# Performance work log

Measured on AMD Instinct MI355X. Metric: run time of the kernel, lower is better.

The kernel has to match this reference:

```python
import jax, jax.numpy as jnp
import numpy as np


def _mlp(x, w1, b1, w2, b2):
    # torch Mlp: fc1 -> GELU (exact erf) -> fc2, dropout off in eval
    h = jax.nn.gelu(x @ w1 + b1, approximate=False)
    return h @ w2 + b2


def _nearest(x, oh, ow):
    # torch F.interpolate mode='nearest' on [B,h,w,d]: src = floor(dst*in/out)
    h, w = x.shape[1], x.shape[2]
    ih = (np.arange(oh) * h) // oh
    iw = (np.arange(ow) * w) // ow
    return x[:, ih][:, :, iw]


def setup_inputs() -> dict:
    key = jax.random.key(0)
    ks = jax.random.split(key, 8)
    B, s0, dim, nPnt, new2 = 4, 12, 256, 128, 48  # new_size=24
    sc = 0.02
    return {
        "token_init": jax.random.normal(ks[0], (B, s0, s0, dim), jnp.float32),
        "point_token": jax.random.normal(ks[1], (B, nPnt, dim), jnp.float32),
        "nr_w1": jax.random.normal(ks[2], (nPnt, 4 * nPnt), jnp.float32) * sc,
        "nr_b1": jnp.zeros((4 * nPnt,), jnp.float32),
        "nr_w2": jax.random.normal(ks[3], (4 * nPnt, nPnt), jnp.float32) * sc,
        "nr_b2": jnp.zeros((nPnt,), jnp.float32),
        "na_w1": jax.random.normal(ks[4], (nPnt, 4 * nPnt), jnp.float32) * sc,
        "na_b1": jnp.zeros((4 * nPnt,), jnp.float32),
        "na_w2": jax.random.normal(ks[5], (4 * nPnt, nPnt), jnp.float32) * sc,
        "na_b2": jnp.zeros((nPnt,), jnp.float32),
        "tf_w1": jax.random.normal(ks[6], (new2, new2), jnp.float32) * sc,
        "tf_b1": jnp.zeros((new2,), jnp.float32),
        "tf_w2": jax.random.normal(ks[7], (new2, 1), jnp.float32) * sc,
        "tf_b2": jnp.zeros((1,), jnp.float32),
        "height": 120,
        "width": 160,
    }


def reference(token_init, point_token, nr_w1, nr_b1, nr_w2, nr_b2,
              na_w1, na_b1, na_w2, na_b2, tf_w1, tf_b1, tf_w2, tf_b2,
              height, width):
    B, nPnt, dim = point_token.shape
    new_size = tf_w1.shape[0] // 2
    scale = dim ** (-0.5)
    # is_init=False path: repeat_interleave x2 along H and W
    t = jnp.repeat(jnp.repeat(token_init, 2, axis=1), 2, axis=2)  # [B,2s,2s,d]
    token_raw = _nearest(t, height, width)                        # [B,H,W,d]
    t_exp = _nearest(t, new_size, new_size)                       # [B,sH,sW,d]
    sH = sW = new_size
    token_templ = t_exp.reshape(B, sH * sW, dim)
    node_adj = jnp.einsum('bnd,bpd->bnp', token_templ, point_token) * scale
    node_adj = _mlp(node_adj, nr_w1, nr_b1, nr_w2, nr_b2)
    node_adj = node_adj.reshape(B, sH, sW, nPnt)
    node_w = jnp.einsum('bhwp,bhwd->bhpd', node_adj, t_exp) * (sW ** -0.5)
    node_h = jnp.einsum('bhwp,bhwd->bwpd', node_adj, t_exp) * (sH ** -0.5)
    token_n = jnp.concatenate([node_w, node_h], axis=1)           # [B,2s,nPnt,d]
    x = token_n.reshape(B, sH + sW, nPnt * dim).transpose(0, 2, 1)  # [B,nPnt*d,2s]
    token_fused = _mlp(x, tf_w1, tf_b1, tf_w2, tf_b2)             # [B,nPnt*d,1]
    token_fused = token_fused.reshape(B, nPnt, dim)
    token_raw_f = token_raw.reshape(B, height * width, dim)
    node_attn = jnp.einsum('bnd,bpd->bnp', token_raw_f, point_token) * scale
    node_attn = jax.nn.softmax(_mlp(node_attn, na_w1, na_b1, na_w2, na_b2), axis=-1)
    token_new = node_attn @ token_fused + token_raw_f             # [B,HW,d]
    return token_new
```

## Files before the change

kernel.cpp:

```cpp
#include <hip/hip_runtime.h>
#include <math.h>

#define B     4
#define DIM   256
#define NP    128
#define NS    144
#define HID   512
#define NROW  576
#define H_OUT 120
#define W_OUT 160

__device__ __forceinline__ float gelu_exact(float x) {
    return 0.5f * x * (1.0f + erff(x * 0.70710678118654752440f));
}

__global__ __launch_bounds__(256) void k_t(
    const float* __restrict__ pt, float* __restrict__ ptT)
{
    const int bid = blockIdx.x;
    const int b   = bid >> 5;
    const int rem = bid & 31;
    const int d0  = (rem >> 2) * 32;
    const int p0  = (rem & 3) * 32;
    const int t   = threadIdx.x;
    __shared__ float tile[32][33];

    #pragma unroll
    for (int i = t; i < 1024; i += 256) {
        const int row = i >> 5, col = i & 31;
        tile[row][col] = pt[(size_t)(b * NP + p0 + row) * DIM + d0 + col];
    }
    __syncthreads();
    #pragma unroll
    for (int i = t; i < 1024; i += 256) {
        const int row = i >> 5, col = i & 31;
        ptT[(size_t)(b * DIM + d0 + row) * NP + p0 + col] = tile[col][row];
    }
}

__global__ __launch_bounds__(256) void k_mlp(
    const float* __restrict__ ti, const float* __restrict__ ptT,
    const float* __restrict__ nr_w1, const float* __restrict__ nr_b1,
    const float* __restrict__ nr_w2, const float* __restrict__ nr_b2,
    const float* __restrict__ na_w1, const float* __restrict__ na_b1,
    const float* __restrict__ na_w2, const float* __restrict__ na_b2,
    float* __restrict__ nadjT, float* __restrict__ attn)
{
    const int mlp  = blockIdx.x / 144;
    const int tile = blockIdx.x % 144;
    const int g0 = tile * 4;
    const int b  = g0 / NS;
    const int n0 = g0 % NS;
    const int t  = threadIdx.x;

    const float* __restrict__ w1 = mlp ? na_w1 : nr_w1;
    const float* __restrict__ b1 = mlp ? na_b1 : nr_b1;
    const float* __restrict__ w2 = mlp ? na_w2 : nr_w2;
    const float* __restrict__ b2 = mlp ? na_b2 : nr_b2;

    __shared__ float xs[4][DIM];
    __shared__ float parA[2][4][NP];
    __shared__ float qs[4][NP];
    __shared__ float hs[4][HID];
    __shared__ float par[8][4][NP];
    __shared__ float wred[4][2];

    {
        const int r = t >> 6, c = t & 63;
        ((float4*)xs[r])[c] = ((const float4*)ti)[(size_t)(g0 + r) * 64 + c];
    }
    __syncthreads();

    {
        const int pq = t & 31;
        const int rr = (t >> 5) & 3;
        const int dh = t >> 7;
        const float4* __restrict__ pT4 =
            (const float4*)(ptT + (size_t)b * DIM * NP) + pq;
        float4 acc = make_float4(0.f, 0.f, 0.f, 0.f);
        #pragma unroll 8
        for (int d2 = 0; d2 < 128; ++d2) {
            const int d = dh * 128 + d2;
            const float4 v4 = pT4[(size_t)d * 32];
            const float  xv = xs[rr][d];
            acc.x += xv * v4.x; acc.y += xv * v4.y;
            acc.z += xv * v4.z; acc.w += xv * v4.w;
        }
        ((float4*)parA[dh][rr])[pq] = acc;
    }
    __syncthreads();

    const int p  = t & 127;
    const int rh = t >> 7;
    qs[rh][p]     = (parA[0][rh][p]     + parA[1][rh][p])     * 0.0625f;
    qs[rh + 2][p] = (parA[0][rh + 2][p] + parA[1][rh + 2][p]) * 0.0625f;
    __syncthreads();

    {
        const int kq = t & 127;
        const int k0 = kq * 4;
        float4 acc0 = *(const float4*)(b1 + k0);
        float4 acc1 = acc0;
        const float* __restrict__ wp = w1 + k0;
        #pragma unroll 16
        for (int pp = 0; pp < NP; ++pp) {
            const float4 w4 = *(const float4*)(wp + (size_t)pp * HID);
            const float q0 = qs[rh][pp];
            const float q1 = qs[rh + 2][pp];
            acc0.x += q0*w4.x; acc0.y += q0*w4.y;
            acc0.z += q0*w4.z; acc0.w += q0*w4.w;
            acc1.x += q1*w4.x; acc1.y += q1*w4.y;
            acc1.z += q1*w4.z; acc1.w += q1*w4.w;
        }
        float4 o0, o1;
        o0.x = gelu_exact(acc0.x); o0.y = gelu_exact(acc0.y);
        o0.z = gelu_exact(acc0.z); o0.w = gelu_exact(acc0.w);
        o1.x = gelu_exact(acc1.x); o1.y = gelu_exact(acc1.y);
        o1.z = gelu_exact(acc1.z); o1.w = gelu_exact(acc1.w);
        ((float4*)hs[rh])[kq]     = o0;
        ((float4*)hs[rh + 2])[kq] = o1;
    }
    __syncthreads();

    {
        const int pq = t & 31;
        const int p0 = pq * 4;
        const int kg = t >> 5;
        float4 a0 = make_float4(0.f,0.f,0.f,0.f);
        float4 a1 = a0, a2 = a0, a3 = a0;
        const float4* __restrict__ w24 = (const float4*)(w2 + p0);
        #pragma unroll 8
        for (int i = 0; i < 64; ++i) {
            const int k = kg * 64 + i;
            const float4 w4 = w24[(size_t)k * 32];
            const float h0 = hs[0][k], h1 = hs[1][k];
            const float h2 = hs[2][k], h3 = hs[3][k];
            a0.x += h0*w4.x; a0.y += h0*w4.y; a0.z += h0*w4.z; a0.w += h0*w4.w;
            a1.x += h1*w4.x; a1.y += h1*w4.y; a1.z += h1*w4.z; a1.w += h1*w4.w;
            a2.x += h2*w4.x; a2.y += h2*w4.y; a2.z += h2*w4.z; a2.w += h2*w4.w;
            a3.x += h3*w4.x; a3.y += h3*w4.y; a3.z += h3*w4.z; a3.w += h3*w4.w;
        }
        ((float4*)par[kg][0])[pq] = a0;
        ((float4*)par[kg][1])[pq] = a1;
        ((float4*)par[kg][2])[pq] = a2;
        ((float4*)par[kg][3])[pq] = a3;
    }
    __syncthreads();

    float lg0 = b2[p], lg1 = lg0;
    #pragma unroll
    for (int kg = 0; kg < 8; ++kg) {
        lg0 += par[kg][rh][p];
        lg1 += par[kg][rh + 2][p];
    }

    if (mlp == 0) {
        float* __restrict__ dst = nadjT + (size_t)(b * NP + p) * NS + n0;
        dst[rh]     = lg0;
        dst[rh + 2] = lg1;
    } else {
        const int wid   = t >> 6;
        const int wpair = wid ^ 1;
        float m0 = lg0, m1 = lg1;
        #pragma unroll
        for (int off = 32; off > 0; off >>= 1) {
            m0 = fmaxf(m0, __shfl_xor(m0, off));
            m1 = fmaxf(m1, __shfl_xor(m1, off));
        }
        if ((t & 63) == 0) { wred[wid][0] = m0; wred[wid][1] = m1; }
        __syncthreads();
        m0 = fmaxf(m0, wred[wpair][0]);
        m1 = fmaxf(m1, wred[wpair][1]);

        const float e0 = expf(lg0 - m0), e1 = expf(lg1 - m1);
        float s0 = e0, s1 = e1;
        #pragma unroll
        for (int off = 32; off > 0; off >>= 1) {
            s0 += __shfl_xor(s0, off);
            s1 += __shfl_xor(s1, off);
        }
        __syncthreads();
        if ((t & 63) == 0) { wred[wid][0] = s0; wred[wid][1] = s1; }
        __syncthreads();
        s0 += wred[wpair][0];
        s1 += wred[wpair][1];

        attn[(size_t)(g0 + rh) * NP + p]     = e0 / s0;
        attn[(size_t)(g0 + rh + 2) * NP + p] = e1 / s1;
    }
}

__global__ __launch_bounds__(256) void k_fold(
    const float* __restrict__ nadjT, const float* __restrict__ ti,
    const float* __restrict__ w1, const float* __restrict__ b1,
    const float* __restrict__ w2, const float* __restrict__ b2,
    float* __restrict__ tf)
{
    const int b = blockIdx.x >> 7;
    const int p = blockIdx.x & 127;
    const int t = threadIdx.x;
    __shared__ float an[NS];
    __shared__ float w1p[24][48];
    __shared__ float b1s[48];
    __shared__ float w2s[48];

    if (t < 36) {
        ((float4*)an)[t] =
            ((const float4*)(nadjT + (size_t)(b * NP + p) * NS))[t];
    }
    if (t >= 192 && t < 240) {
        const int k = t - 192;
        b1s[k] = b1[k];
        w2s[k] = w2[k];
    }
    for (int i = t; i < 24 * 48; i += 256) {
        const int m = i / 48, k = i - m * 48;
        w1p[m][k] = w1[(2 * m) * 48 + k] + w1[(2 * m + 1) * 48 + k];
    }
    __syncthreads();

    const int d = t;
    const float* __restrict__ tb = ti + (size_t)b * NS * DIM + d;
    float v[24];
    #pragma unroll
    for (int m = 0; m < 24; ++m) v[m] = 0.f;
    #pragma unroll
    for (int y = 0; y < 12; ++y) {
        #pragma unroll
        for (int x = 0; x < 12; ++x) {
            const int n = y * 12 + x;
            const float tv = tb[n * DIM];
            const float a  = an[n];
            v[y]      += a * tv;
            v[12 + x] += a * tv;
        }
    }
    const float c = 0.40824829046386301637f;
    #pragma unroll
    for (int m = 0; m < 24; ++m) v[m] *= c;

    float acc = b2[0];
    for (int k = 0; k < 48; ++k) {
        float tt = b1s[k];
        #pragma unroll
        for (int m = 0; m < 24; ++m) tt += v[m] * w1p[m][k];
        acc += gelu_exact(tt) * w2s[k];
    }
    tf[(size_t)(b * NP + p) * DIM + d] = acc;
}

__global__ __launch_bounds__(256) void k_final(
    const float* __restrict__ attn, const float* __restrict__ tf,
    const float* __restrict__ ti, float4* __restrict__ out)
{
    const int g = blockIdx.x;
    const int b = g / NS;
    const int n = g % NS;
    const int t = threadIdx.x;
    const int dq = t & 63;
    const int pg = t >> 6;

    __shared__ float  at[NP];
    __shared__ float4 par4[4][64];
    __shared__ float4 rowf[64];

    if (t < NP) at[t] = attn[(size_t)g * NP + t];
    __syncthreads();

    const float4* __restrict__ tp = (const float4*)tf + (size_t)b * NP * 64 + dq;
    float4 acc = make_float4(0.f, 0.f, 0.f, 0.f);
    #pragma unroll 16
    for (int i = 0; i < 32; ++i) {
        const int pp = pg * 32 + i;
        const float  a  = at[pp];
        const float4 tv = tp[(size_t)pp * 64];
        acc.x += a * tv.x; acc.y += a * tv.y;
        acc.z += a * tv.z; acc.w += a * tv.w;
    }
    par4[pg][dq] = acc;
    __syncthreads();

    if (t < 64) {
        float4 s = par4[0][t];
        const float4 s1 = par4[1][t], s2 = par4[2][t], s3 = par4[3][t];
        const float4 tiv = ((const float4*)ti)[(size_t)g * 64 + t];
        s.x += s1.x + s2.x + s3.x + tiv.x;
        s.y += s1.y + s2.y + s3.y + tiv.y;
        s.z += s1.z + s2.z + s3.z + tiv.z;
        s.w += s1.w + s2.w + s3.w + tiv.w;
        rowf[t] = s;
    }
    __syncthreads();

    const int y = n / 12, x = n % 12;
    const int w_lo = (40 * x + 2) / 3;
    const int w_hi = (40 * x + 42) / 3;
    const float4 val = rowf[dq];
    const int h0 = 10 * y;
    for (int h = h0; h < h0 + 10; ++h) {
        float4* __restrict__ orow = out + (size_t)((b * H_OUT + h) * W_OUT) * 64 + dq;
        for (int w = w_lo + pg; w < w_hi; w += 4) {
            orow[(size_t)w * 64] = val;
        }
    }
}

extern "C" void kernel_launch(void* const* d_in, const int* in_sizes, int n_in,
                              void* d_out, int out_size, void* d_ws, size_t ws_size,
                              hipStream_t stream) {
    (void)in_sizes; (void)n_in; (void)out_size; (void)ws_size;
    const float* token_init  = (const float*)d_in[0];
    const float* point_token = (const float*)d_in[1];
    const float* nr_w1 = (const float*)d_in[2];
    const float* nr_b1 = (const float*)d_in[3];
    const float* nr_w2 = (const float*)d_in[4];
    const float* nr_b2 = (const float*)d_in[5];
    const float* na_w1 = (const float*)d_in[6];
    const float* na_b1 = (const float*)d_in[7];
    const float* na_w2 = (const float*)d_in[8];
    const float* na_b2 = (const float*)d_in[9];
    const float* tf_w1 = (const float*)d_in[10];
    const float* tf_b1 = (const float*)d_in[11];
    const float* tf_w2 = (const float*)d_in[12];
    const float* tf_b2 = (const float*)d_in[13];

    float* out = (float*)d_out;
    float* ws  = (float*)d_ws;
    float* nadjT = ws;
    float* attn  = nadjT + NROW * NP;
    float* tf    = attn + NROW * NP;
    float* ptT   = tf + B * NP * DIM;

    k_t<<<128, 256, 0, stream>>>(point_token, ptT);
    k_mlp<<<288, 256, 0, stream>>>(token_init, ptT,
                                   nr_w1, nr_b1, nr_w2, nr_b2,
                                   na_w1, na_b1, na_w2, na_b2,
                                   nadjT, attn);
    k_fold<<<B * NP, 256, 0, stream>>>(nadjT, token_init,
                                       tf_w1, tf_b1, tf_w2, tf_b2, tf);
    k_final<<<NROW, 256, 0, stream>>>(attn, tf, token_init, (float4*)out);
}
```

Measured before the change: 166.9 us.

## Precompute folded tf_w1 once and register-block the score GEMV over rows

The row-pair sum of tf_w1 used by k_fold is now computed once by an extra block in the transpose kernel and stored in workspace. This replaces the 512 per-block shared-memory rebuilds, and k_fold now reads weights, biases and node_adj straight from global memory with no barrier. In k_mlp the point-token score product now has each thread compute all 4 rows over a 32-wide slice of d, so each ptT float4 load is reused across 4 rows. The cost is an 8-way partial reduction instead of a 2-way one. The global weight reads in k_fold go through cache instead of shared memory, which may add latency in the inner GELU loop.

Measured after the change: 160.7 us. -3.7%, faster.

```diff
diff --git a/kernel.cpp b/kernel.cpp
--- a/kernel.cpp
+++ b/kernel.cpp
@@ -15,14 +15,24 @@
 }
 
 __global__ __launch_bounds__(256) void k_t(
-    const float* __restrict__ pt, float* __restrict__ ptT)
+    const float* __restrict__ pt, const float* __restrict__ tf_w1,
+    float* __restrict__ ptT, float* __restrict__ w1pg)
 {
     const int bid = blockIdx.x;
+    const int t   = threadIdx.x;
+
+    if (bid == 128) {
+        for (int i = t; i < 24 * 48; i += 256) {
+            const int m = i / 48, k = i - m * 48;
+            w1pg[i] = tf_w1[(2 * m) * 48 + k] + tf_w1[(2 * m + 1) * 48 + k];
+        }
+        return;
+    }
+
     const int b   = bid >> 5;
     const int rem = bid & 31;
     const int d0  = (rem >> 2) * 32;
     const int p0  = (rem & 3) * 32;
-    const int t   = threadIdx.x;
     __shared__ float tile[32][33];
 
     #pragma unroll
@@ -59,7 +69,7 @@
     const float* __restrict__ b2 = mlp ? na_b2 : nr_b2;
 
     __shared__ float xs[4][DIM];
-    __shared__ float parA[2][4][NP];
+    __shared__ float parA[8][4][NP];
     __shared__ float qs[4][NP];
     __shared__ float hs[4][HID];
     __shared__ float par[8][4][NP];
@@ -73,27 +83,41 @@
 
     {
         const int pq = t & 31;
-        const int rr = (t >> 5) & 3;
-        const int dh = t >> 7;
+        const int dg = t >> 5;
         const float4* __restrict__ pT4 =
             (const float4*)(ptT + (size_t)b * DIM * NP) + pq;
-        float4 acc = make_float4(0.f, 0.f, 0.f, 0.f);
+        float4 a0 = make_float4(0.f,0.f,0.f,0.f);
+        float4 a1 = a0, a2 = a0, a3 = a0;
         #pragma unroll 8
-        for (int d2 = 0; d2 < 128; ++d2) {
-            const int d = dh * 128 + d2;
+        for (int d2 = 0; d2 < 32; ++d2) {
+            const int d = dg * 32 + d2;
             const float4 v4 = pT4[(size_t)d * 32];
-            const float  xv = xs[rr][d];
-            acc.x += xv * v4.x; acc.y += xv * v4.y;
-            acc.z += xv * v4.z; acc.w += xv * v4.w;
-        }
-        ((float4*)parA[dh][rr])[pq] = acc;
+            const float x0 = xs[0][d], x1 = xs[1][d];
+            const float x2 = xs[2][d], x3 = xs[3][d];
+            a0.x += x0*v4.x; a0.y += x0*v4.y; a0.z += x0*v4.z; a0.w += x0*v4.w;
+            a1.x += x1*v4.x; a1.y += x1*v4.y; a1.z += x1*v4.z; a1.w += x1*v4.w;
+            a2.x += x2*v4.x; a2.y += x2*v4.y; a2.z += x2*v4.z; a2.w += x2*v4.w;
+            a3.x += x3*v4.x; a3.y += x3*v4.y; a3.z += x3*v4.z; a3.w += x3*v4.w;
+        }
+        ((float4*)parA[dg][0])[pq] = a0;
+        ((float4*)parA[dg][1])[pq] = a1;
+        ((float4*)parA[dg][2])[pq] = a2;
+        ((float4*)parA[dg][3])[pq] = a3;
     }
     __syncthreads();
 
     const int p  = t & 127;
     const int rh = t >> 7;
-    qs[rh][p]     = (parA[0][rh][p]     + parA[1][rh][p])     * 0.0625f;
-    qs[rh + 2][p] = (parA[0][rh + 2][p] + parA[1][rh + 2][p]) * 0.0625f;
+    {
+        float q0 = 0.f, q1 = 0.f;
+        #pragma unroll
+        for (int dg = 0; dg < 8; ++dg) {
+            q0 += parA[dg][rh][p];
+            q1 += parA[dg][rh + 2][p];
+        }
+        qs[rh][p]     = q0 * 0.0625f;
+        qs[rh + 2][p] = q1 * 0.0625f;
+    }
     __syncthreads();
 
     {
@@ -192,35 +216,18 @@
 
 __global__ __launch_bounds__(256) void k_fold(
     const float* __restrict__ nadjT, const float* __restrict__ ti,
-    const float* __restrict__ w1, const float* __restrict__ b1,
-    const float* __restrict__ w2, const float* __restrict__ b2,
-    float* __restrict__ tf)
+    const float* __restrict__ w1p,
+    const float* __restrict__ b1, const float* __restrict__ w2,
+    const float* __restrict__ b2, float* __restrict__ tf)
 {
     const int b = blockIdx.x >> 7;
     const int p = blockIdx.x & 127;
     const int t = threadIdx.x;
-    __shared__ float an[NS];
-    __shared__ float w1p[24][48];
-    __shared__ float b1s[48];
-    __shared__ float w2s[48];
-
-    if (t < 36) {
-        ((float4*)an)[t] =
-            ((const float4*)(nadjT + (size_t)(b * NP + p) * NS))[t];
-    }
-    if (t >= 192 && t < 240) {
-        const int k = t - 192;
-        b1s[k] = b1[k];
-        w2s[k] = w2[k];
-    }
-    for (int i = t; i < 24 * 48; i += 256) {
-        const int m = i / 48, k = i - m * 48;
-        w1p[m][k] = w1[(2 * m) * 48 + k] + w1[(2 * m + 1) * 48 + k];
-    }
-    __syncthreads();
-
+
+    const float* __restrict__ an = nadjT + (size_t)(b * NP + p) * NS;
     const int d = t;
     const float* __restrict__ tb = ti + (size_t)b * NS * DIM + d;
+
     float v[24];
     #pragma unroll
     for (int m = 0; m < 24; ++m) v[m] = 0.f;
@@ -241,10 +248,10 @@
 
     float acc = b2[0];
     for (int k = 0; k < 48; ++k) {
-        float tt = b1s[k];
-        #pragma unroll
-        for (int m = 0; m < 24; ++m) tt += v[m] * w1p[m][k];
-        acc += gelu_exact(tt) * w2s[k];
+        float tt = b1[k];
+        #pragma unroll
+        for (int m = 0; m < 24; ++m) tt += v[m] * w1p[m * 48 + k];
+        acc += gelu_exact(tt) * w2[k];
     }
     tf[(size_t)(b * NP + p) * DIM + d] = acc;
 }
@@ -330,13 +337,14 @@
     float* attn  = nadjT + NROW * NP;
     float* tf    = attn + NROW * NP;
     float* ptT   = tf + B * NP * DIM;
-
-    k_t<<<128, 256, 0, stream>>>(point_token, ptT);
+    float* w1pg  = ptT + B * DIM * NP;
+
+    k_t<<<129, 256, 0, stream>>>(point_token, tf_w1, ptT, w1pg);
     k_mlp<<<288, 256, 0, stream>>>(token_init, ptT,
                                    nr_w1, nr_b1, nr_w2, nr_b2,
                                    na_w1, na_b1, na_w2, na_b2,
                                    nadjT, attn);
-    k_fold<<<B * NP, 256, 0, stream>>>(nadjT, token_init,
-                                       tf_w1, tf_b1, tf_w2, tf_b2, tf);
+    k_fold<<<B * NP, 256, 0, stream>>>(nadjT, token_init, w1pg,
+                                       tf_b1, tf_w2, tf_b2, tf);
     k_final<<<NROW, 256, 0, stream>>>(attn, tf, token_init, (float4*)out);
 }
```
